# Optimization experiments

Hardware: AMD Instinct MI355X
Metric: run time of the kernel (lower is better)

Reference implementation:

```python
import jax, jax.numpy as jnp
import numpy as np

L = 4        # num_layers
B = 32       # batch
N = 512      # num_nodes == seq_len
D = 256      # d_model
H = 8        # nhead
HD = D // H  # head_dim
F = 1024     # dim_feedforward
EPS = 1e-5


def setup_inputs() -> dict:
    key = jax.random.key(0)
    ks = jax.random.split(key, 12)
    w = lambda k, shape: jax.random.normal(k, shape, jnp.float32) * 0.02
    return {
        "src": jax.random.normal(ks[0], (B, N, D), jnp.float32),
        # node embeddings (torch.randn -> std 1)
        "e1": jax.random.normal(ks[1], (N, D), jnp.float32),
        "e2": jax.random.normal(ks[2], (N, D), jnp.float32),
        # per-layer attention projections, stored [L, d_in, d_out]
        "Wq": w(ks[3], (L, D, D)), "bq": jnp.zeros((L, D), jnp.float32),
        "Wk": w(ks[4], (L, D, D)), "bk": jnp.zeros((L, D), jnp.float32),
        "Wv": w(ks[5], (L, D, D)), "bv": jnp.zeros((L, D), jnp.float32),
        "Wo": w(ks[6], (L, D, D)), "bo": jnp.zeros((L, D), jnp.float32),
        # FFN
        "W1": w(ks[7], (L, D, F)), "b1": jnp.zeros((L, F), jnp.float32),
        "W2": w(ks[8], (L, F, D)), "b2": jnp.zeros((L, D), jnp.float32),
        # LayerNorms
        "g1": jnp.ones((L, D), jnp.float32), "be1": jnp.zeros((L, D), jnp.float32),
        "g2": jnp.ones((L, D), jnp.float32), "be2": jnp.zeros((L, D), jnp.float32),
    }


def _layernorm(x, g, b):
    mu = jnp.mean(x, axis=-1, keepdims=True)
    var = jnp.mean(jnp.square(x - mu), axis=-1, keepdims=True)
    return (x - mu) * jax.lax.rsqrt(var + EPS) * g + b


def reference(src, e1, e2, Wq, bq, Wk, bk, Wv, bv, Wo, bo,
              W1, b1, W2, b2, g1, be1, g2, be2):
    # adaptive spatial bias shared across all layers: [N, N]
    bias = jnp.matmul(e1, e2.T)
    scale = 1.0 / jnp.sqrt(jnp.float32(HD))
    x = src
    for l in range(L):
        def heads(t):  # [B,N,D] -> [B,H,N,HD]
            return t.reshape(B, N, H, HD).transpose(0, 2, 1, 3)
        q = heads(x @ Wq[l] + bq[l])
        k = heads(x @ Wk[l] + bk[l])
        v = heads(x @ Wv[l] + bv[l])
        # scores + shared additive bias (broadcast over batch and heads)
        scores = jnp.einsum('bhqd,bhkd->bhqk', q, k) * scale + bias
        attn = jax.nn.softmax(scores, axis=-1)
        o = jnp.einsum('bhqk,bhkd->bhqd', attn, v)
        o = o.transpose(0, 2, 1, 3).reshape(B, N, D) @ Wo[l] + bo[l]
        x = _layernorm(x + o, g1[l], be1[l])
        ff = jax.nn.relu(x @ W1[l] + b1[l]) @ W2[l] + b2[l]
        x = _layernorm(x + ff, g2[l], be2[l])
    return x
```

## Files before the change

### kernel.cpp

```cpp
#include <hip/hip_runtime.h>

typedef __bf16 bf16;
typedef __bf16 v8bf __attribute__((ext_vector_type(8)));
typedef float  v4f  __attribute__((ext_vector_type(4)));
typedef float  v16f __attribute__((ext_vector_type(16)));
typedef unsigned short u16;
typedef u16 v8us __attribute__((ext_vector_type(8)));
typedef unsigned int v4u __attribute__((ext_vector_type(4)));

#define L_ 4
#define B_ 32
#define N_ 512
#define D_ 256
#define H_ 8
#define F_ 1024
#define ROWS (B_*N_)
#define QHSZ ((size_t)B_*H_*N_*32)

__device__ __forceinline__ void gload16(const void* g, void* l) {
  __builtin_amdgcn_global_load_lds((__attribute__((address_space(1))) void*)g,
                                   (__attribute__((address_space(3))) void*)l,
                                   16, 0, 0);
}

__device__ __forceinline__ unsigned pk_bf16(float a, float b) {
  unsigned r;
  asm("v_cvt_pk_bf16_f32 %0, %1, %2" : "=v"(r) : "v"(a), "v"(b));
  return r;
}

#define PLSWAP(a, b) asm volatile("v_permlane32_swap_b32 %0, %1" : "+v"(a), "+v"(b))

#define EXP2(x) __builtin_amdgcn_exp2f(x)

template <int N> __device__ __forceinline__ void waitvm() {
  if constexpr (N == 0) asm volatile("s_waitcnt vmcnt(0)" ::: "memory");
  else if constexpr (N == 2) asm volatile("s_waitcnt vmcnt(2)" ::: "memory");
  else if constexpr (N == 3) asm volatile("s_waitcnt vmcnt(3)" ::: "memory");
  else if constexpr (N == 4) asm volatile("s_waitcnt vmcnt(4)" ::: "memory");
  else if constexpr (N == 5) asm volatile("s_waitcnt vmcnt(5)" ::: "memory");
  else if constexpr (N == 6) asm volatile("s_waitcnt vmcnt(6)" ::: "memory");
}

__global__ __launch_bounds__(256) void bias_gemm(
    const float* __restrict__ e1, const float* __restrict__ e2,
    float* __restrict__ biasP) {
  __shared__ float As[16][16];
  __shared__ float Bs[16][16];
  const int tx = threadIdx.x, ty = threadIdx.y;
  const int r = blockIdx.y * 16 + ty, c = blockIdx.x * 16 + tx;
  float acc = 0.f;
  for (int k0 = 0; k0 < D_; k0 += 16) {
    As[ty][tx] = e1[r * D_ + k0 + tx];
    Bs[ty][tx] = e2[(blockIdx.x * 16 + ty) * D_ + k0 + tx];
    __syncthreads();
#pragma unroll
    for (int kk = 0; kk < 16; ++kk) acc += As[ty][kk] * Bs[tx][kk];
    __syncthreads();
  }
  const int kb = r >> 5, r5 = r & 31;
  const int blk = kb * 8 + (r5 >> 3) * 2 + ((r5 >> 2) & 1);
  biasP[(size_t)(blk * 512 + c) * 4 + (r5 & 3)] = acc * 1.4426950408889634f;
}

__global__ __launch_bounds__(256) void colmax(
    const float* __restrict__ biasP, float* __restrict__ mq) {
  const int q = blockIdx.x * 256 + threadIdx.x;
  float mx = -1e30f;
  for (int blk = 0; blk < 128; ++blk) {
    const float4 v = *(const float4*)&biasP[(size_t)(blk * 512 + q) * 4];
    mx = fmaxf(mx, fmaxf(fmaxf(v.x, v.y), fmaxf(v.z, v.w)));
  }
  mq[q] = mx;
}

__global__ __launch_bounds__(256) void subm(
    float* __restrict__ biasP, const float* __restrict__ mq) {
  const int i = blockIdx.x * 256 + threadIdx.x;
  float4 v = ((float4*)biasP)[i];
  const float m = mq[i & 511];
  v.x -= m; v.y -= m; v.z -= m; v.w -= m;
  ((float4*)biasP)[i] = v;
}

__global__ __launch_bounds__(256) void convT(
    const float* __restrict__ W, bf16* __restrict__ Wt,
    int K, int N, size_t inL, size_t outL) {
  __shared__ float t[32][33];
  const int l = blockIdx.z;
  const int k0 = blockIdx.y * 32, n0 = blockIdx.x * 32;
  const int r = threadIdx.x >> 5, c = threadIdx.x & 31;
#pragma unroll
  for (int i = 0; i < 4; ++i)
    t[r + 8 * i][c] = W[l * inL + (size_t)(k0 + r + 8 * i) * N + n0 + c];
  __syncthreads();
#pragma unroll
  for (int i = 0; i < 4; ++i)
    Wt[l * outL + (size_t)(n0 + r + 8 * i) * K + k0 + c] = (bf16)t[c][r + 8 * i];
}

__global__ __launch_bounds__(256) void pack_bqkv(
    const float* __restrict__ bq, const float* __restrict__ bk,
    const float* __restrict__ bv, float* __restrict__ bqkv) {
  const int i = blockIdx.x * 256 + threadIdx.x;
  if (i < L_ * 768) {
    const int l = i / 768, n = i - l * 768;
    float v = (n < 256) ? bq[l * 256 + n]
            : (n < 512) ? bk[l * 256 + n - 256]
                        : bv[l * 256 + n - 512];
    bqkv[i] = v;
  }
}

__global__ __launch_bounds__(256) void init_x(
    const float* __restrict__ src, bf16* __restrict__ xb) {
  const int i = blockIdx.x * 256 + threadIdx.x;
  float4 v = ((const float4*)src)[i];
  uint2 w;
  w.x = pk_bf16(v.x, v.y);
  w.y = pk_bf16(v.z, v.w);
  ((uint2*)xb)[i] = w;
}

template <int BM, int BN, int WPC, int RELU, int OUTMODE, int RESID>
__global__ __launch_bounds__(256, WPC) void gemm_bf16k(
    const bf16* __restrict__ A, const bf16* __restrict__ Bt,
    const float* __restrict__ bias, const bf16* __restrict__ resid,
    void* __restrict__ Cout, int M, int N, int K, int nbx) {
  constexpr int MR = BM / 32, NR = BN / 32;
  constexpr int NSLAB = (BM + BN) / 16;
  constexpr int LPW = NSLAB / 4;
  constexpr int BUFE = (BM + BN) * 32;
  __shared__ __align__(16) bf16 lds[3 * BUFE];
  const int tid  = threadIdx.x;
  const int wave = tid >> 6, lane = tid & 63;
  const int l15 = lane & 15, l4 = lane >> 4;
  const int qq = gridDim.x >> 3;
  const int wg = (blockIdx.x & 7) * qq + (blockIdx.x >> 3);
  const int bx = wg % nbx, by = wg / nbx;
  const int bm = by * BM, bn = bx * BN;
  const int wr = (wave >> 1) * (BM / 2), wc = (wave & 1) * (BN / 2);
  const int lrow = lane >> 2;
  const int lk   = (lane & 3) * 8;

  v4f acc[MR][NR];
#pragma unroll
  for (int m = 0; m < MR; ++m)
#pragma unroll
    for (int n = 0; n < NR; ++n) acc[m][n] = (v4f){0.f, 0.f, 0.f, 0.f};

  auto STAGE = [&](int buf, int k0) {
    bf16* dst = &lds[buf * BUFE];
#pragma unroll
    for (int s = wave; s < NSLAB; s += 4) {
      if (s < BM / 16)
        gload16(A + (size_t)(bm + s * 16 + lrow) * K + k0 + lk, dst + s * 512);
      else
        gload16(Bt + (size_t)(bn + (s - BM / 16) * 16 + lrow) * K + k0 + lk, dst + s * 512);
    }
  };

  const int nk = K >> 5;
  STAGE(0, 0);
  STAGE(1, 32);
  waitvm<LPW>();
  __builtin_amdgcn_s_barrier();
  __builtin_amdgcn_sched_barrier(0);

  int cur = 0;
  for (int t = 0; t < nk; ++t) {
    const bool pf = (t + 2 < nk);
    if (pf) STAGE(cur == 0 ? 2 : cur - 1, (t + 2) * 32);
    const bf16* buf = &lds[cur * BUFE];
    v8bf af[MR], bfr[NR];
#pragma unroll
    for (int m = 0; m < MR; ++m)
      af[m] = *(const v8bf*)&buf[(wr + m * 16 + l15) * 32 + l4 * 8];
#pragma unroll
    for (int n = 0; n < NR; ++n)
      bfr[n] = *(const v8bf*)&buf[BM * 32 + (wc + n * 16 + l15) * 32 + l4 * 8];
    __builtin_amdgcn_s_setprio(1);
#pragma unroll
    for (int m = 0; m < MR; ++m)
#pragma unroll
      for (int n = 0; n < NR; ++n)
        acc[m][n] = __builtin_amdgcn_mfma_f32_16x16x32_bf16(af[m], bfr[n], acc[m][n], 0, 0, 0);
    __builtin_amdgcn_s_setprio(0);
    if (pf) waitvm<LPW>();
    else    waitvm<0>();
    __builtin_amdgcn_s_barrier();
    __builtin_amdgcn_sched_barrier(0);
    cur = (cur == 2) ? 0 : cur + 1;
  }

#pragma unroll
  for (int m = 0; m < MR; ++m) {
    const int row0 = bm + wr + m * 16 + l4 * 4;
#pragma unroll
    for (int n = 0; n < NR; ++n) {
      const int col = bn + wc + n * 16 + l15;
      const float bc = bias[col];
      if constexpr (OUTMODE == 2) {
        const int sec = col >> 8, hh = (col >> 5) & 7, d = col & 31;
        const int bb = row0 >> 9, nr0 = row0 & 511;
        bf16* dst = (bf16*)Cout + (size_t)sec * QHSZ +
                    (((size_t)bb * 8 + hh) * 512 + nr0) * 32 + d;
#pragma unroll
        for (int i = 0; i < 4; ++i)
          dst[i * 32] = (bf16)(acc[m][n][i] + bc);
      } else {
#pragma unroll
        for (int i = 0; i < 4; ++i) {
          const size_t idx = (size_t)(row0 + i) * N + col;
          float v = acc[m][n][i] + bc;
          if (RESID) v += (float)resid[idx];
          if (RELU) v = fmaxf(v, 0.f);
          if (OUTMODE == 1) ((bf16*)Cout)[idx] = (bf16)v;
          else              ((float*)Cout)[idx] = v;
        }
      }
    }
  }
}

#define VTS 520
__global__ __launch_bounds__(256, 3) void attn_k(
    const bf16* __restrict__ qkvh, const float* __restrict__ biasP,
    bf16* __restrict__ outp) {
  __shared__ u16 Vt[32 * VTS];
  const int tid = threadIdx.x;
  const int wave = tid >> 6, lane = tid & 63;
  const int l31 = lane & 31, hi = lane >> 5;
  const int fid = blockIdx.x;
  const int xcd = fid & 7, idx = fid >> 3;
  const int b = (xcd << 2) | (idx >> 5);
  const int h = (idx & 31) >> 2;
  const int qblk = idx & 3;
  const u16* Qh = (const u16*)qkvh + (((size_t)b * 8 + h) * 512) * 32;
  const u16* Kh = Qh + QHSZ;
  const u16* Vh = Qh + 2 * QHSZ;
  const int qb = qblk * 128 + wave * 32;

  {
    const u16* p0 = Vh + (size_t)(2 * tid) * 32;
    const u16* p1 = p0 + 32;
#pragma unroll
    for (int d0 = 0; d0 < 32; d0 += 8) {
      v8us a = *(const v8us*)(p0 + d0);
      v8us c = *(const v8us*)(p1 + d0);
#pragma unroll
      for (int j = 0; j < 8; ++j) {
        unsigned u = (unsigned)a[j] | ((unsigned)c[j] << 16);
        *(unsigned*)&Vt[(d0 + j) * VTS + tid * 2] = u;
      }
    }
  }
  __syncthreads();

  const u16* qrow = Qh + (size_t)(qb + l31) * 32;
  const v8bf qf0 = *(const v8bf*)(qrow + hi * 8);
  const v8bf qf1 = *(const v8bf*)(qrow + 16 + hi * 8);
  const float* bpl = biasP + ((size_t)(hi * 512 + qb + l31)) * 4;

  const float SC2 = 0.17677669529663688f * 1.4426950408889634f;
  float lsum = 0.f;
  v16f accO = {0.f,0.f,0.f,0.f,0.f,0.f,0.f,0.f,0.f,0.f,0.f,0.f,0.f,0.f,0.f,0.f};

  v8bf ka0 = *(const v8bf*)(Kh + (size_t)l31 * 32 + hi * 8);
  v8bf ka1 = *(const v8bf*)(Kh + (size_t)l31 * 32 + 16 + hi * 8);
  v4f bb[4];
#pragma unroll
  for (int g = 0; g < 4; ++g) bb[g] = *(const v4f*)(bpl + (size_t)(g * 2) * 2048);

  v16f stC = {0.f,0.f,0.f,0.f,0.f,0.f,0.f,0.f,0.f,0.f,0.f,0.f,0.f,0.f,0.f,0.f};
  stC = __builtin_amdgcn_mfma_f32_32x32x16_bf16(ka0, qf0, stC, 0, 0, 0);
  stC = __builtin_amdgcn_mfma_f32_32x32x16_bf16(ka1, qf1, stC, 0, 0, 0);
  {
    const u16* kn = Kh + (size_t)(32 + l31) * 32;
    ka0 = *(const v8bf*)(kn + hi * 8);
    ka1 = *(const v8bf*)(kn + 16 + hi * 8);
  }

  for (int kb = 0; kb < 16; ++kb) {
    const int kbase = kb * 32;
    v16f stN = {0.f,0.f,0.f,0.f,0.f,0.f,0.f,0.f,0.f,0.f,0.f,0.f,0.f,0.f,0.f,0.f};
    __builtin_amdgcn_s_setprio(1);
    stN = __builtin_amdgcn_mfma_f32_32x32x16_bf16(ka0, qf0, stN, 0, 0, 0);
    stN = __builtin_amdgcn_mfma_f32_32x32x16_bf16(ka1, qf1, stN, 0, 0, 0);
    __builtin_amdgcn_s_setprio(0);

    const u16* kn = Kh + (size_t)(kbase + 64 + l31) * 32;
    const v8bf kn0 = *(const v8bf*)(kn + hi * 8);
    const v8bf kn1 = *(const v8bf*)(kn + 16 + hi * 8);
    v4f bn[4];
#pragma unroll
    for (int g = 0; g < 4; ++g)
      bn[g] = *(const v4f*)(bpl + (size_t)((kb + 1) * 8 + g * 2) * 2048);

    float p[16];
#pragma unroll
    for (int r = 0; r < 16; ++r)
      p[r] = EXP2(stC[r] * SC2 + bb[r >> 2][r & 3]);

    float s8[8], s4[4];
#pragma unroll
    for (int r = 0; r < 8; ++r) s8[r] = p[r] + p[r + 8];
#pragma unroll
    for (int r = 0; r < 4; ++r) s4[r] = s8[r] + s8[r + 4];
    lsum += (s4[0] + s4[2]) + (s4[1] + s4[3]);

    unsigned u[8];
#pragma unroll
    for (int t = 0; t < 8; ++t) u[t] = pk_bf16(p[2 * t], p[2 * t + 1]);
    PLSWAP(u[0], u[2]);
    PLSWAP(u[1], u[3]);
    PLSWAP(u[4], u[6]);
    PLSWAP(u[5], u[7]);
    union { v4u u; v8bf h; } cv0, cv1;
    cv0.u = (v4u){u[0], u[1], u[2], u[3]};
    cv1.u = (v4u){u[4], u[5], u[6], u[7]};

    const v8bf va0 = *(const v8bf*)&Vt[l31 * VTS + kbase + hi * 8];
    const v8bf va1 = *(const v8bf*)&Vt[l31 * VTS + kbase + 16 + hi * 8];
    __builtin_amdgcn_s_setprio(1);
    accO = __builtin_amdgcn_mfma_f32_32x32x16_bf16(va0, cv0.h, accO, 0, 0, 0);
    accO = __builtin_amdgcn_mfma_f32_32x32x16_bf16(va1, cv1.h, accO, 0, 0, 0);
    __builtin_amdgcn_s_setprio(0);

    stC = stN;
    ka0 = kn0; ka1 = kn1;
#pragma unroll
    for (int g = 0; g < 4; ++g) bb[g] = bn[g];
  }

  lsum += __shfl_xor(lsum, 32);

  const float inv = 1.0f / lsum;
  u16* orow = (u16*)outp + (size_t)(b * N_ + qb + l31) * D_ + h * 32 + 4 * hi;
#pragma unroll
  for (int g = 0; g < 4; ++g) {
    uint2 w;
    w.x = pk_bf16(accO[4 * g] * inv, accO[4 * g + 1] * inv);
    w.y = pk_bf16(accO[4 * g + 2] * inv, accO[4 * g + 3] * inv);
    *(uint2*)(orow + 8 * g) = w;
  }
}

template <int WF32>
__global__ __launch_bounds__(256) void ln_kernel(
    const float* __restrict__ xin,
    const float* __restrict__ g, const float* __restrict__ b,
    float* __restrict__ xout_f32, bf16* __restrict__ xbout) {
  const int wv = threadIdx.x >> 6, ln = threadIdx.x & 63;
  const size_t row = blockIdx.x * 4 + wv;
  const size_t o4 = row * D_ + ln * 4;
  const float4 v = *(const float4*)&xin[o4];
  float s  = (v.x + v.y) + (v.z + v.w);
  float ss = (v.x * v.x + v.y * v.y) + (v.z * v.z + v.w * v.w);
#pragma unroll
  for (int off = 1; off < 64; off <<= 1) {
    s  += __shfl_xor(s, off);
    ss += __shfl_xor(ss, off);
  }
  const float mu = s * (1.f / D_);
  const float var = ss * (1.f / D_) - mu * mu;
  const float rs = rsqrtf(var + 1e-5f);
  const float4 gg = *(const float4*)&g[ln * 4];
  const float4 bb = *(const float4*)&b[ln * 4];
  float4 o;
  o.x = (v.x - mu) * rs * gg.x + bb.x;
  o.y = (v.y - mu) * rs * gg.y + bb.y;
  o.z = (v.z - mu) * rs * gg.z + bb.z;
  o.w = (v.w - mu) * rs * gg.w + bb.w;
  if constexpr (WF32) {
    *(float4*)&xout_f32[o4] = o;
  } else {
    uint2 w;
    w.x = pk_bf16(o.x, o.y);
    w.y = pk_bf16(o.z, o.w);
    *(uint2*)&xbout[o4] = w;
  }
}

extern "C" void kernel_launch(void* const* d_in, const int* in_sizes, int n_in,
                              void* d_out, int out_size, void* d_ws, size_t ws_size,
                              hipStream_t stream) {
  const float* src = (const float*)d_in[0];
  const float* e1  = (const float*)d_in[1];
  const float* e2  = (const float*)d_in[2];
  const float* Wq  = (const float*)d_in[3];
  const float* bq  = (const float*)d_in[4];
  const float* Wk  = (const float*)d_in[5];
  const float* bk  = (const float*)d_in[6];
  const float* Wv  = (const float*)d_in[7];
  const float* bv  = (const float*)d_in[8];
  const float* Wo  = (const float*)d_in[9];
  const float* bo  = (const float*)d_in[10];
  const float* W1  = (const float*)d_in[11];
  const float* b1  = (const float*)d_in[12];
  const float* W2  = (const float*)d_in[13];
  const float* b2  = (const float*)d_in[14];
  const float* g1  = (const float*)d_in[15];
  const float* be1 = (const float*)d_in[16];
  const float* g2  = (const float*)d_in[17];
  const float* be2 = (const float*)d_in[18];

  char* ws = (char*)d_ws;
  size_t off = 0;
  auto alloc = [&](size_t bytes) {
    void* p = ws + off;
    off += (bytes + 255) & ~(size_t)255;
    return p;
  };
  float* biasP  = (float*)alloc((size_t)2 * 1024 * 1024);
  float* mq     = (float*)alloc((size_t)N_ * 4);
  bf16*  xb     = (bf16*) alloc((size_t)ROWS * D_ * 2);
  bf16*  attn_o = (bf16*) alloc((size_t)ROWS * D_ * 2);
  float* tmp    = (float*)alloc((size_t)ROWS * D_ * 4);
  bf16*  qkvh   = (bf16*) alloc((size_t)ROWS * 1024 * 2 + 65536);
  bf16*  h1     = qkvh;
  bf16*  Wqkvt  = (bf16*) alloc((size_t)L_ * 768 * 256 * 2);
  bf16*  Wot    = (bf16*) alloc((size_t)L_ * 256 * 256 * 2);
  bf16*  W1t    = (bf16*) alloc((size_t)L_ * 1024 * 256 * 2);
  bf16*  W2t    = (bf16*) alloc((size_t)L_ * 256 * 1024 * 2);
  float* bqkv   = (float*)alloc((size_t)L_ * 768 * 4);

  bias_gemm<<<dim3(32, 32), dim3(16, 16), 0, stream>>>(e2, e1, biasP);
  colmax<<<2, 256, 0, stream>>>(biasP, mq);
  subm<<<256, 256, 0, stream>>>(biasP, mq);
  convT<<<dim3(8, 8, L_),  256, 0, stream>>>(Wq, Wqkvt,          256, 256, 65536, 196608);
  convT<<<dim3(8, 8, L_),  256, 0, stream>>>(Wk, Wqkvt + 65536,  256, 256, 65536, 196608);
  convT<<<dim3(8, 8, L_),  256, 0, stream>>>(Wv, Wqkvt + 131072, 256, 256, 65536, 196608);
  convT<<<dim3(8, 8, L_),  256, 0, stream>>>(Wo, Wot,            256, 256, 65536, 65536);
  convT<<<dim3(32, 8, L_), 256, 0, stream>>>(W1, W1t, 256, 1024, 262144, 262144);
  convT<<<dim3(8, 32, L_), 256, 0, stream>>>(W2, W2t, 1024, 256, 262144, 262144);
  pack_bqkv<<<12, 256, 0, stream>>>(bq, bk, bv, bqkv);
  init_x<<<ROWS * D_ / 1024, 256, 0, stream>>>(src, xb);

  for (int l = 0; l < L_; ++l) {
    gemm_bf16k<128, 128, 3, 0, 2, 0><<<768, 256, 0, stream>>>(
        xb, Wqkvt + (size_t)l * 196608, bqkv + l * 768, nullptr, qkvh,
        ROWS, 768, 256, 6);
    attn_k<<<1024, 256, 0, stream>>>(qkvh, biasP, attn_o);
    gemm_bf16k<64, 128, 4, 0, 0, 1><<<512, 256, 0, stream>>>(
        attn_o, Wot + (size_t)l * 65536, bo + l * 256, xb, tmp,
        ROWS, 256, 256, 2);
    ln_kernel<0><<<ROWS / 4, 256, 0, stream>>>(tmp, g1 + l * 256, be1 + l * 256, nullptr, xb);
    gemm_bf16k<128, 256, 2, 1, 1, 0><<<512, 256, 0, stream>>>(
        xb, W1t + (size_t)l * 262144, b1 + l * 1024, nullptr, h1,
        ROWS, 1024, 256, 4);
    gemm_bf16k<64, 128, 4, 0, 0, 1><<<512, 256, 0, stream>>>(
        h1, W2t + (size_t)l * 262144, b2 + l * 256, xb, tmp,
        ROWS, 256, 1024, 2);
    if (l == L_ - 1)
      ln_kernel<1><<<ROWS / 4, 256, 0, stream>>>(tmp, g2 + l * 256, be2 + l * 256, (float*)d_out, nullptr);
    else
      ln_kernel<0><<<ROWS / 4, 256, 0, stream>>>(tmp, g2 + l * 256, be2 + l * 256, nullptr, xb);
  }
}
```

Before: 487.3 us.

## Fuse output-projection and FFN2 GEMMs with residual add and LayerNorm

Adds a gemmln kernel that computes a 32-row by 256-column tile, so each workgroup owns complete rows. It adds bias and residual, reduces row statistics across waves through shared memory, and writes the normalized bf16 (or final fp32) output directly. This removes the fp32 temp buffer round trip and the separate LayerNorm launches. In exchange, the tiles are narrower in M (32 rows) with a 3-stage LDS pipeline, which may lower GEMM efficiency compared with the previous 64x128 tiling.

```diff
diff --git a/kernel.cpp b/kernel.cpp
--- a/kernel.cpp
+++ b/kernel.cpp
@@ -223,6 +223,145 @@
   }
 }
 
+template <int WF32>
+__global__ __launch_bounds__(256, 2) void gemmln(
+    const bf16* __restrict__ A, const bf16* __restrict__ Bt,
+    const float* __restrict__ bias,
+    const float* __restrict__ g, const float* __restrict__ be,
+    bf16* __restrict__ xb, float* __restrict__ outf32, int K) {
+  constexpr int NSLAB = 18;
+  constexpr int BUFE = NSLAB * 512;
+  __shared__ __align__(16) bf16 lds[3 * BUFE];
+  __shared__ float redS[4][32], redSS[4][32];
+  const int tid  = threadIdx.x;
+  const int wave = tid >> 6, lane = tid & 63;
+  const int l15 = lane & 15, l4 = lane >> 4;
+  const int qq = gridDim.x >> 3;
+  const int wg = (blockIdx.x & 7) * qq + (blockIdx.x >> 3);
+  const int bm = wg * 32;
+  const int wc = wave * 64;
+  const int lrow = lane >> 2;
+  const int lk   = (lane & 3) * 8;
+
+  v4f acc[2][4];
+#pragma unroll
+  for (int m = 0; m < 2; ++m)
+#pragma unroll
+    for (int n = 0; n < 4; ++n) acc[m][n] = (v4f){0.f, 0.f, 0.f, 0.f};
+
+  auto STAGE = [&](int buf, int k0) {
+    bf16* dst = &lds[buf * BUFE];
+    for (int s = wave; s < NSLAB; s += 4) {
+      if (s < 2)
+        gload16(A + (size_t)(bm + s * 16 + lrow) * K + k0 + lk, dst + s * 512);
+      else
+        gload16(Bt + (size_t)((s - 2) * 16 + lrow) * K + k0 + lk, dst + s * 512);
+    }
+  };
+
+  const int nk = K >> 5;
+  STAGE(0, 0);
+  STAGE(1, 32);
+  waitvm<4>();
+  __builtin_amdgcn_s_barrier();
+  __builtin_amdgcn_sched_barrier(0);
+
+  int cur = 0;
+  for (int t = 0; t < nk; ++t) {
+    const bool pf = (t + 2 < nk);
+    if (pf) STAGE(cur == 0 ? 2 : cur - 1, (t + 2) * 32);
+    const bf16* buf = &lds[cur * BUFE];
+    v8bf af[2], bfr[4];
+#pragma unroll
+    for (int m = 0; m < 2; ++m)
+      af[m] = *(const v8bf*)&buf[(m * 16 + l15) * 32 + l4 * 8];
+#pragma unroll
+    for (int n = 0; n < 4; ++n)
+      bfr[n] = *(const v8bf*)&buf[1024 + (wc + n * 16 + l15) * 32 + l4 * 8];
+    __builtin_amdgcn_s_setprio(1);
+#pragma unroll
+    for (int m = 0; m < 2; ++m)
+#pragma unroll
+      for (int n = 0; n < 4; ++n)
+        acc[m][n] = __builtin_amdgcn_mfma_f32_16x16x32_bf16(af[m], bfr[n], acc[m][n], 0, 0, 0);
+    __builtin_amdgcn_s_setprio(0);
+    if (pf) waitvm<4>();
+    else    waitvm<0>();
+    __builtin_amdgcn_s_barrier();
+    __builtin_amdgcn_sched_barrier(0);
+    cur = (cur == 2) ? 0 : cur + 1;
+  }
+
+  float s[2][4], ss[2][4];
+#pragma unroll
+  for (int m = 0; m < 2; ++m)
+#pragma unroll
+    for (int i = 0; i < 4; ++i) { s[m][i] = 0.f; ss[m][i] = 0.f; }
+#pragma unroll
+  for (int m = 0; m < 2; ++m) {
+    const int row0 = bm + m * 16 + l4 * 4;
+#pragma unroll
+    for (int n = 0; n < 4; ++n) {
+      const int col = wc + n * 16 + l15;
+      const float bc = bias[col];
+#pragma unroll
+      for (int i = 0; i < 4; ++i) {
+        const size_t idx = (size_t)(row0 + i) * 256 + col;
+        const float v = acc[m][n][i] + bc + (float)xb[idx];
+        acc[m][n][i] = v;
+        s[m][i] += v; ss[m][i] += v * v;
+      }
+    }
+  }
+#pragma unroll
+  for (int off = 1; off < 16; off <<= 1)
+#pragma unroll
+    for (int m = 0; m < 2; ++m)
+#pragma unroll
+      for (int i = 0; i < 4; ++i) {
+        s[m][i]  += __shfl_xor(s[m][i], off);
+        ss[m][i] += __shfl_xor(ss[m][i], off);
+      }
+  if (l15 == 0) {
+#pragma unroll
+    for (int m = 0; m < 2; ++m)
+#pragma unroll
+      for (int i = 0; i < 4; ++i) {
+        redS[wave][m * 16 + l4 * 4 + i]  = s[m][i];
+        redSS[wave][m * 16 + l4 * 4 + i] = ss[m][i];
+      }
+  }
+  __syncthreads();
+  float mu[2][4], rs[2][4];
+#pragma unroll
+  for (int m = 0; m < 2; ++m)
+#pragma unroll
+    for (int i = 0; i < 4; ++i) {
+      const int r = m * 16 + l4 * 4 + i;
+      const float S  = redS[0][r] + redS[1][r] + redS[2][r] + redS[3][r];
+      const float SS = redSS[0][r] + redSS[1][r] + redSS[2][r] + redSS[3][r];
+      mu[m][i] = S * (1.f / 256.f);
+      const float var = SS * (1.f / 256.f) - mu[m][i] * mu[m][i];
+      rs[m][i] = rsqrtf(var + 1e-5f);
+    }
+#pragma unroll
+  for (int m = 0; m < 2; ++m) {
+    const int row0 = bm + m * 16 + l4 * 4;
+#pragma unroll
+    for (int n = 0; n < 4; ++n) {
+      const int col = wc + n * 16 + l15;
+      const float gc = g[col], bec = be[col];
+#pragma unroll
+      for (int i = 0; i < 4; ++i) {
+        const size_t idx = (size_t)(row0 + i) * 256 + col;
+        const float o = (acc[m][n][i] - mu[m][i]) * rs[m][i] * gc + bec;
+        if (WF32) outf32[idx] = o;
+        else      xb[idx] = (bf16)o;
+      }
+    }
+  }
+}
+
 #define VTS 520
 __global__ __launch_bounds__(256, 3) void attn_k(
     const bf16* __restrict__ qkvh, const float* __restrict__ biasP,
@@ -343,42 +482,6 @@
     w.x = pk_bf16(accO[4 * g] * inv, accO[4 * g + 1] * inv);
     w.y = pk_bf16(accO[4 * g + 2] * inv, accO[4 * g + 3] * inv);
     *(uint2*)(orow + 8 * g) = w;
-  }
-}
-
-template <int WF32>
-__global__ __launch_bounds__(256) void ln_kernel(
-    const float* __restrict__ xin,
-    const float* __restrict__ g, const float* __restrict__ b,
-    float* __restrict__ xout_f32, bf16* __restrict__ xbout) {
-  const int wv = threadIdx.x >> 6, ln = threadIdx.x & 63;
-  const size_t row = blockIdx.x * 4 + wv;
-  const size_t o4 = row * D_ + ln * 4;
-  const float4 v = *(const float4*)&xin[o4];
-  float s  = (v.x + v.y) + (v.z + v.w);
-  float ss = (v.x * v.x + v.y * v.y) + (v.z * v.z + v.w * v.w);
-#pragma unroll
-  for (int off = 1; off < 64; off <<= 1) {
-    s  += __shfl_xor(s, off);
-    ss += __shfl_xor(ss, off);
-  }
-  const float mu = s * (1.f / D_);
-  const float var = ss * (1.f / D_) - mu * mu;
-  const float rs = rsqrtf(var + 1e-5f);
-  const float4 gg = *(const float4*)&g[ln * 4];
-  const float4 bb = *(const float4*)&b[ln * 4];
-  float4 o;
-  o.x = (v.x - mu) * rs * gg.x + bb.x;
-  o.y = (v.y - mu) * rs * gg.y + bb.y;
-  o.z = (v.z - mu) * rs * gg.z + bb.z;
-  o.w = (v.w - mu) * rs * gg.w + bb.w;
-  if constexpr (WF32) {
-    *(float4*)&xout_f32[o4] = o;
-  } else {
-    uint2 w;
-    w.x = pk_bf16(o.x, o.y);
-    w.y = pk_bf16(o.z, o.w);
-    *(uint2*)&xbout[o4] = w;
   }
 }
 
@@ -416,7 +519,6 @@
   float* mq     = (float*)alloc((size_t)N_ * 4);
   bf16*  xb     = (bf16*) alloc((size_t)ROWS * D_ * 2);
   bf16*  attn_o = (bf16*) alloc((size_t)ROWS * D_ * 2);
-  float* tmp    = (float*)alloc((size_t)ROWS * D_ * 4);
   bf16*  qkvh   = (bf16*) alloc((size_t)ROWS * 1024 * 2 + 65536);
   bf16*  h1     = qkvh;
   bf16*  Wqkvt  = (bf16*) alloc((size_t)L_ * 768 * 256 * 2);
@@ -442,19 +544,19 @@
         xb, Wqkvt + (size_t)l * 196608, bqkv + l * 768, nullptr, qkvh,
         ROWS, 768, 256, 6);
     attn_k<<<1024, 256, 0, stream>>>(qkvh, biasP, attn_o);
-    gemm_bf16k<64, 128, 4, 0, 0, 1><<<512, 256, 0, stream>>>(
-        attn_o, Wot + (size_t)l * 65536, bo + l * 256, xb, tmp,
-        ROWS, 256, 256, 2);
-    ln_kernel<0><<<ROWS / 4, 256, 0, stream>>>(tmp, g1 + l * 256, be1 + l * 256, nullptr, xb);
+    gemmln<0><<<512, 256, 0, stream>>>(
+        attn_o, Wot + (size_t)l * 65536, bo + l * 256,
+        g1 + l * 256, be1 + l * 256, xb, nullptr, 256);
     gemm_bf16k<128, 256, 2, 1, 1, 0><<<512, 256, 0, stream>>>(
         xb, W1t + (size_t)l * 262144, b1 + l * 1024, nullptr, h1,
         ROWS, 1024, 256, 4);
-    gemm_bf16k<64, 128, 4, 0, 0, 1><<<512, 256, 0, stream>>>(
-        h1, W2t + (size_t)l * 262144, b2 + l * 256, xb, tmp,
-        ROWS, 256, 1024, 2);
     if (l == L_ - 1)
-      ln_kernel<1><<<ROWS / 4, 256, 0, stream>>>(tmp, g2 + l * 256, be2 + l * 256, (float*)d_out, nullptr);
+      gemmln<1><<<512, 256, 0, stream>>>(
+          h1, W2t + (size_t)l * 262144, b2 + l * 256,
+          g2 + l * 256, be2 + l * 256, xb, (float*)d_out, 1024);
     else
-      ln_kernel<0><<<ROWS / 4, 256, 0, stream>>>(tmp, g2 + l * 256, be2 + l * 256, nullptr, xb);
-  }
-}
+      gemmln<0><<<512, 256, 0, stream>>>(
+          h1, W2t + (size_t)l * 262144, b2 + l * 256,
+          g2 + l * 256, be2 + l * 256, xb, nullptr, 1024);
+  }
+}
```

Result: no change. 495.0 us (+1.6%).
